# Optimization experiments

Hardware: AMD Instinct MI355X
Metric: run time of the kernel (lower is better)

The kernel has to match this reference:

```python
import jax, jax.numpy as jnp
import numpy as np


def setup_inputs() -> dict:
    key = jax.random.key(0)
    kx, ky, kz = jax.random.split(key, 3)
    x = jax.random.normal(kx, (32, 2048, 1024), dtype=jnp.float32)
    y = jax.random.normal(ky, (8, 32, 2048, 64), dtype=jnp.float32)
    z = jax.random.normal(kz, (32, 4096, 512), dtype=jnp.float32)
    return {"x": x, "y": y, "z": z}


def reference(x, y, z):
    # torch.topk(x, 4): top-4 largest along last dim, sorted descending
    x_top, _ = jax.lax.top_k(x, 4)  # [32, 2048, 4]

    # torch.topk(y, k=1, dim=2, largest=False): single smallest along dim 2.
    # Move dim 2 to last, take top-1 of the negation, negate back.
    y_m = jnp.moveaxis(y, 2, -1)              # [8, 32, 64, 2048]
    y_min = -jax.lax.top_k(-y_m, 1)[0]        # [8, 32, 64, 1]
    y_min = jnp.moveaxis(y_min, -1, 2)        # [8, 32, 1, 64]

    # torch.topk(z, k=3, dim=-1, sorted=False): top-3 values + indices.
    # (sorted=False allows any order; we return them sorted descending,
    # which is a valid ordering of the same selected set.)
    z_top, z_idx = jax.lax.top_k(z, 3)        # [32, 4096, 3] each

    return (x_top, y_min, z_top, z_idx)
```

## Files before the change

### kernel.cpp

```cpp
#include <hip/hip_runtime.h>

#define OUT_X  0
#define OUT_Y  262144
#define OUT_ZV 278528
#define OUT_ZI 671744

#define YB 256
#define ZB 32768
#define XB 16384

typedef float vf4 __attribute__((ext_vector_type(4)));

__device__ __forceinline__ float4 ldnt4(const float4* p) {
    vf4 v = __builtin_nontemporal_load((const vf4*)p);
    return make_float4(v.x, v.y, v.z, v.w);
}


__device__ __forceinline__ void bub4(float &a0, float &a1, float &a2, float &a3, float v) {
    float r;
    r = fminf(a0, v); a0 = fmaxf(a0, v); v = r;
    r = fminf(a1, v); a1 = fmaxf(a1, v); v = r;
    r = fminf(a2, v); a2 = fmaxf(a2, v); v = r;
    a3 = fmaxf(a3, v);
}

__device__ __forceinline__ void merge4(float &a0, float &a1, float &a2, float &a3,
                                       float b0, float b1, float b2, float b3) {
    float m0 = fmaxf(a0, b3), m1 = fmaxf(a1, b2), m2 = fmaxf(a2, b1), m3 = fmaxf(a3, b0);
    float e0 = fmaxf(m0, m2), e2 = fminf(m0, m2);
    float e1 = fmaxf(m1, m3), e3 = fminf(m1, m3);
    a0 = fmaxf(e0, e1); a1 = fminf(e0, e1);
    a2 = fmaxf(e2, e3); a3 = fminf(e2, e3);
}


__device__ __forceinline__ float4 min4(float4 a, float4 b) {
    return make_float4(fminf(a.x, b.x), fminf(a.y, b.y), fminf(a.z, b.z), fminf(a.w, b.w));
}


__device__ __forceinline__ unsigned long long mkkey(float v, int idx) {
    unsigned int b = __float_as_uint(v);
    unsigned int u = b ^ ((unsigned int)((int)b >> 31) | 0x80000000u);
    return ((unsigned long long)u << 32) | (unsigned int)(511 - idx);
}

__device__ __forceinline__ void ins3(unsigned long long &k0, unsigned long long &k1,
                                     unsigned long long &k2, unsigned long long k) {
    unsigned long long t;
    t = (k0 > k) ? k : k0; k0 = (k0 > k) ? k0 : k; k = t;
    t = (k1 > k) ? k : k1; k1 = (k1 > k) ? k1 : k; k = t;
    k2 = (k2 > k) ? k2 : k;
}

__device__ __forceinline__ void ce64(unsigned long long &a, unsigned long long &b) {
    unsigned long long hi = (a > b) ? a : b;
    unsigned long long lo = (a > b) ? b : a;
    a = hi; b = lo;
}

__device__ __forceinline__ void merge3(unsigned long long &a0, unsigned long long &a1,
                                       unsigned long long &a2,
                                       unsigned long long b0, unsigned long long b1,
                                       unsigned long long b2) {
    unsigned long long m0 = (a0 > b2) ? a0 : b2;
    unsigned long long m1 = (a1 > b1) ? a1 : b1;
    unsigned long long m2 = (a2 > b0) ? a2 : b0;
    ce64(m0, m1); ce64(m1, m2); ce64(m0, m1);
    a0 = m0; a1 = m1; a2 = m2;
}

__device__ __forceinline__ unsigned long long shfl_xor_u64(unsigned long long v, int mask) {
    unsigned int lo = (unsigned int)v;
    unsigned int hi = (unsigned int)(v >> 32);
    lo = __shfl_xor(lo, mask, 64);
    hi = __shfl_xor(hi, mask, 64);
    return ((unsigned long long)hi << 32) | lo;
}


__global__ __launch_bounds__(256) void fused_topk_kernel(const float* __restrict__ x,
                                                         const float* __restrict__ y,
                                                         const float* __restrict__ z,
                                                         float* __restrict__ out) {
    const int bid = blockIdx.x;
    const int tid = threadIdx.x;

    if (bid < YB) {
        const int pair = bid;
        const int c4 = tid & 15;
        const int rg = tid >> 4;
        const float4* base = (const float4*)(y + (size_t)pair * 2048 * 64);

        const float INF = 3.402823466e38f;
        float4 m = make_float4(INF, INF, INF, INF);
        #pragma unroll 8
        for (int r = rg; r < 2048; r += 16) {
            m = min4(m, ldnt4(base + r * 16 + c4));
        }

        __shared__ float4 red[256];
        red[tid] = m;
        __syncthreads();
        #pragma unroll
        for (int s = 128; s >= 16; s >>= 1) {
            if (tid < s) red[tid] = min4(red[tid], red[tid + s]);
            __syncthreads();
        }
        if (tid < 16) {
            ((float4*)(out + OUT_Y + pair * 64))[tid] = red[tid];
        }
    } else if (bid < YB + ZB) {
        const int lane = tid & 63;
        const int row  = (bid - YB) * 4 + (tid >> 6);
        const float4* r4 = (const float4*)(z + (size_t)row * 512);

        float4 v0 = ldnt4(r4 + lane);
        float4 v1 = ldnt4(r4 + lane + 64);

        unsigned long long a0 = 0ull, a1 = 0ull, a2 = 0ull;
        unsigned long long b0 = 0ull, b1 = 0ull, b2 = 0ull;
        int i0 = 4 * lane, i1 = 4 * (lane + 64);
        ins3(a0, a1, a2, mkkey(v0.x, i0));
        ins3(b0, b1, b2, mkkey(v1.x, i1));
        ins3(a0, a1, a2, mkkey(v0.y, i0 + 1));
        ins3(b0, b1, b2, mkkey(v1.y, i1 + 1));
        ins3(a0, a1, a2, mkkey(v0.z, i0 + 2));
        ins3(b0, b1, b2, mkkey(v1.z, i1 + 2));
        ins3(a0, a1, a2, mkkey(v0.w, i0 + 3));
        ins3(b0, b1, b2, mkkey(v1.w, i1 + 3));
        merge3(a0, a1, a2, b0, b1, b2);

        #pragma unroll
        for (int m = 1; m < 64; m <<= 1) {
            unsigned long long s0 = shfl_xor_u64(a0, m);
            unsigned long long s1 = shfl_xor_u64(a1, m);
            unsigned long long s2 = shfl_xor_u64(a2, m);
            merge3(a0, a1, a2, s0, s1, s2);
        }

        if (lane == 0) {
            unsigned long long ks[3] = {a0, a1, a2};
            float* outv = out + OUT_ZV;
            float* outi = out + OUT_ZI;
            #pragma unroll
            for (int j = 0; j < 3; ++j) {
                unsigned int u = (unsigned int)(ks[j] >> 32);
                unsigned int bb = (u & 0x80000000u) ? (u ^ 0x80000000u) : ~u;
                outv[(size_t)row * 3 + j] = __uint_as_float(bb);
                outi[(size_t)row * 3 + j] = (float)(511 - (int)(ks[j] & 0xFFFFFFFFu));
            }
        }
    } else {
        const int lane = tid & 63;
        const int row  = (bid - YB - ZB) * 4 + (tid >> 6);
        const float4* r4 = (const float4*)(x + (size_t)row * 1024);

        float4 v0 = ldnt4(r4 + lane);
        float4 v1 = ldnt4(r4 + lane + 64);
        float4 v2 = ldnt4(r4 + lane + 128);
        float4 v3 = ldnt4(r4 + lane + 192);

        const float NINF = -3.402823466e38f;
        float a0 = NINF, a1 = NINF, a2 = NINF, a3 = NINF;
        float c0 = NINF, c1 = NINF, c2 = NINF, c3 = NINF;
        bub4(a0, a1, a2, a3, v0.x); bub4(c0, c1, c2, c3, v2.x);
        bub4(a0, a1, a2, a3, v0.y); bub4(c0, c1, c2, c3, v2.y);
        bub4(a0, a1, a2, a3, v0.z); bub4(c0, c1, c2, c3, v2.z);
        bub4(a0, a1, a2, a3, v0.w); bub4(c0, c1, c2, c3, v2.w);
        bub4(a0, a1, a2, a3, v1.x); bub4(c0, c1, c2, c3, v3.x);
        bub4(a0, a1, a2, a3, v1.y); bub4(c0, c1, c2, c3, v3.y);
        bub4(a0, a1, a2, a3, v1.z); bub4(c0, c1, c2, c3, v3.z);
        bub4(a0, a1, a2, a3, v1.w); bub4(c0, c1, c2, c3, v3.w);
        merge4(a0, a1, a2, a3, c0, c1, c2, c3);

        #pragma unroll
        for (int m = 1; m < 64; m <<= 1) {
            float s0 = __shfl_xor(a0, m, 64);
            float s1 = __shfl_xor(a1, m, 64);
            float s2 = __shfl_xor(a2, m, 64);
            float s3 = __shfl_xor(a3, m, 64);
            merge4(a0, a1, a2, a3, s0, s1, s2, s3);
        }

        if (lane == 0) {
            ((float4*)(out + OUT_X))[row] = make_float4(a0, a1, a2, a3);
        }
    }
}

extern "C" void kernel_launch(void* const* d_in, const int* in_sizes, int n_in,
                              void* d_out, int out_size, void* d_ws, size_t ws_size,
                              hipStream_t stream) {
    const float* x = (const float*)d_in[0];
    const float* y = (const float*)d_in[1];
    const float* z = (const float*)d_in[2];
    float* out = (float*)d_out;

    fused_topk_kernel<<<YB + ZB + XB, 256, 0, stream>>>(x, y, z, out);
}
```

Measured before the change: 560.0 us.

## Use float top-3 with index recovery pass and interleave z/x blocks

The z top-3 path now keeps plain float values instead of packed 64-bit keys, which halves shuffle traffic and replaces 64-bit compares with fminf/fmaxf. Indices are recovered afterwards by three wave-wide min-reductions over matching positions, handling ties with a floor on the previous index. Block scheduling is also interleaved, two z blocks per x block, to mix the two workloads across the GPU. The cost is three extra reduction rounds per row, and NaN or -0/+0 equality handling could differ from the key-based version.

Result: no change. 556.5 us (-0.6%).

```diff
diff --git a/kernel.cpp b/kernel.cpp
--- a/kernel.cpp
+++ b/kernel.cpp
@@ -6,8 +6,7 @@
 #define OUT_ZI 671744
 
 #define YB 256
-#define ZB 32768
-#define XB 16384
+#define NG 16384
 
 typedef float vf4 __attribute__((ext_vector_type(4)));
 
@@ -15,6 +14,8 @@
     vf4 v = __builtin_nontemporal_load((const vf4*)p);
     return make_float4(v.x, v.y, v.z, v.w);
 }
+
+__device__ __forceinline__ int imin(int a, int b) { return a < b ? a : b; }
 
 
 __device__ __forceinline__ void bub4(float &a0, float &a1, float &a2, float &a3, float v) {
@@ -40,43 +41,23 @@
 }
 
 
-__device__ __forceinline__ unsigned long long mkkey(float v, int idx) {
-    unsigned int b = __float_as_uint(v);
-    unsigned int u = b ^ ((unsigned int)((int)b >> 31) | 0x80000000u);
-    return ((unsigned long long)u << 32) | (unsigned int)(511 - idx);
-}
-
-__device__ __forceinline__ void ins3(unsigned long long &k0, unsigned long long &k1,
-                                     unsigned long long &k2, unsigned long long k) {
-    unsigned long long t;
-    t = (k0 > k) ? k : k0; k0 = (k0 > k) ? k0 : k; k = t;
-    t = (k1 > k) ? k : k1; k1 = (k1 > k) ? k1 : k; k = t;
-    k2 = (k2 > k) ? k2 : k;
-}
-
-__device__ __forceinline__ void ce64(unsigned long long &a, unsigned long long &b) {
-    unsigned long long hi = (a > b) ? a : b;
-    unsigned long long lo = (a > b) ? b : a;
+__device__ __forceinline__ void ins3f(float &k0, float &k1, float &k2, float v) {
+    float t;
+    t = fminf(k0, v); k0 = fmaxf(k0, v); v = t;
+    t = fminf(k1, v); k1 = fmaxf(k1, v); v = t;
+    k2 = fmaxf(k2, v);
+}
+
+__device__ __forceinline__ void cef(float &a, float &b) {
+    float hi = fmaxf(a, b), lo = fminf(a, b);
     a = hi; b = lo;
 }
 
-__device__ __forceinline__ void merge3(unsigned long long &a0, unsigned long long &a1,
-                                       unsigned long long &a2,
-                                       unsigned long long b0, unsigned long long b1,
-                                       unsigned long long b2) {
-    unsigned long long m0 = (a0 > b2) ? a0 : b2;
-    unsigned long long m1 = (a1 > b1) ? a1 : b1;
-    unsigned long long m2 = (a2 > b0) ? a2 : b0;
-    ce64(m0, m1); ce64(m1, m2); ce64(m0, m1);
+__device__ __forceinline__ void merge3f(float &a0, float &a1, float &a2,
+                                        float b0, float b1, float b2) {
+    float m0 = fmaxf(a0, b2), m1 = fmaxf(a1, b1), m2 = fmaxf(a2, b0);
+    cef(m0, m1); cef(m1, m2); cef(m0, m1);
     a0 = m0; a1 = m1; a2 = m2;
-}
-
-__device__ __forceinline__ unsigned long long shfl_xor_u64(unsigned long long v, int mask) {
-    unsigned int lo = (unsigned int)v;
-    unsigned int hi = (unsigned int)(v >> 32);
-    lo = __shfl_xor(lo, mask, 64);
-    hi = __shfl_xor(hi, mask, 64);
-    return ((unsigned long long)hi << 32) | lo;
 }
 
 
@@ -111,50 +92,77 @@
         if (tid < 16) {
             ((float4*)(out + OUT_Y + pair * 64))[tid] = red[tid];
         }
-    } else if (bid < YB + ZB) {
+        return;
+    }
+
+    const unsigned b = (unsigned)(bid - YB);
+    const unsigned g = b / 3u;
+    const unsigned r3 = b - g * 3u;
+
+    if (r3 < 2u) {
+        const int zb   = (int)(2u * g + r3);
         const int lane = tid & 63;
-        const int row  = (bid - YB) * 4 + (tid >> 6);
+        const int row  = zb * 4 + (tid >> 6);
         const float4* r4 = (const float4*)(z + (size_t)row * 512);
 
-        float4 v0 = ldnt4(r4 + lane);
-        float4 v1 = ldnt4(r4 + lane + 64);
-
-        unsigned long long a0 = 0ull, a1 = 0ull, a2 = 0ull;
-        unsigned long long b0 = 0ull, b1 = 0ull, b2 = 0ull;
-        int i0 = 4 * lane, i1 = 4 * (lane + 64);
-        ins3(a0, a1, a2, mkkey(v0.x, i0));
-        ins3(b0, b1, b2, mkkey(v1.x, i1));
-        ins3(a0, a1, a2, mkkey(v0.y, i0 + 1));
-        ins3(b0, b1, b2, mkkey(v1.y, i1 + 1));
-        ins3(a0, a1, a2, mkkey(v0.z, i0 + 2));
-        ins3(b0, b1, b2, mkkey(v1.z, i1 + 2));
-        ins3(a0, a1, a2, mkkey(v0.w, i0 + 3));
-        ins3(b0, b1, b2, mkkey(v1.w, i1 + 3));
-        merge3(a0, a1, a2, b0, b1, b2);
+        float4 p = ldnt4(r4 + lane);
+        float4 q = ldnt4(r4 + lane + 64);
+
+        const float NINF = -3.402823466e38f;
+        float a0 = NINF, a1 = NINF, a2 = NINF;
+        float b0 = NINF, b1 = NINF, b2 = NINF;
+        ins3f(a0, a1, a2, p.x); ins3f(b0, b1, b2, q.x);
+        ins3f(a0, a1, a2, p.y); ins3f(b0, b1, b2, q.y);
+        ins3f(a0, a1, a2, p.z); ins3f(b0, b1, b2, q.z);
+        ins3f(a0, a1, a2, p.w); ins3f(b0, b1, b2, q.w);
+        merge3f(a0, a1, a2, b0, b1, b2);
 
         #pragma unroll
         for (int m = 1; m < 64; m <<= 1) {
-            unsigned long long s0 = shfl_xor_u64(a0, m);
-            unsigned long long s1 = shfl_xor_u64(a1, m);
-            unsigned long long s2 = shfl_xor_u64(a2, m);
-            merge3(a0, a1, a2, s0, s1, s2);
-        }
+            float s0 = __shfl_xor(a0, m, 64);
+            float s1 = __shfl_xor(a1, m, 64);
+            float s2 = __shfl_xor(a2, m, 64);
+            merge3f(a0, a1, a2, s0, s1, s2);
+        }
+
+        const int gA = 4 * lane;
+        const int BIG = 0x7fffffff;
+
+        #define ZROUND(T, FLOOR, WOUT)                                               \
+        {                                                                            \
+            const float t_ = (T); const int fl_ = (FLOOR);                           \
+            int cand = BIG;                                                          \
+            cand = imin(cand, (p.x == t_ && (gA + 0)   > fl_) ? (gA + 0)   : BIG);   \
+            cand = imin(cand, (p.y == t_ && (gA + 1)   > fl_) ? (gA + 1)   : BIG);   \
+            cand = imin(cand, (p.z == t_ && (gA + 2)   > fl_) ? (gA + 2)   : BIG);   \
+            cand = imin(cand, (p.w == t_ && (gA + 3)   > fl_) ? (gA + 3)   : BIG);   \
+            cand = imin(cand, (q.x == t_ && (gA + 256) > fl_) ? (gA + 256) : BIG);   \
+            cand = imin(cand, (q.y == t_ && (gA + 257) > fl_) ? (gA + 257) : BIG);   \
+            cand = imin(cand, (q.z == t_ && (gA + 258) > fl_) ? (gA + 258) : BIG);   \
+            cand = imin(cand, (q.w == t_ && (gA + 259) > fl_) ? (gA + 259) : BIG);   \
+            _Pragma("unroll")                                                        \
+            for (int m = 1; m < 64; m <<= 1) {                                       \
+                cand = imin(cand, __shfl_xor(cand, m, 64));                          \
+            }                                                                        \
+            WOUT = cand;                                                             \
+        }
+
+        int w0, w1, w2;
+        ZROUND(a0, -1, w0);
+        ZROUND(a1, (a1 == a0) ? w0 : -1, w1);
+        ZROUND(a2, (a2 == a1) ? w1 : -1, w2);
+        #undef ZROUND
 
         if (lane == 0) {
-            unsigned long long ks[3] = {a0, a1, a2};
-            float* outv = out + OUT_ZV;
-            float* outi = out + OUT_ZI;
-            #pragma unroll
-            for (int j = 0; j < 3; ++j) {
-                unsigned int u = (unsigned int)(ks[j] >> 32);
-                unsigned int bb = (u & 0x80000000u) ? (u ^ 0x80000000u) : ~u;
-                outv[(size_t)row * 3 + j] = __uint_as_float(bb);
-                outi[(size_t)row * 3 + j] = (float)(511 - (int)(ks[j] & 0xFFFFFFFFu));
-            }
+            float* outv = out + OUT_ZV + (size_t)row * 3;
+            float* outi = out + OUT_ZI + (size_t)row * 3;
+            outv[0] = a0; outv[1] = a1; outv[2] = a2;
+            outi[0] = (float)w0; outi[1] = (float)w1; outi[2] = (float)w2;
         }
     } else {
+        const int xb   = (int)g;
         const int lane = tid & 63;
-        const int row  = (bid - YB - ZB) * 4 + (tid >> 6);
+        const int row  = xb * 4 + (tid >> 6);
         const float4* r4 = (const float4*)(x + (size_t)row * 1024);
 
         float4 v0 = ldnt4(r4 + lane);
@@ -198,5 +206,5 @@
     const float* z = (const float*)d_in[2];
     float* out = (float*)d_out;
 
-    fused_topk_kernel<<<YB + ZB + XB, 256, 0, stream>>>(x, y, z, out);
-}
+    fused_topk_kernel<<<YB + 3 * NG, 256, 0, stream>>>(x, y, z, out);
+}
```
